# Optimization experiments

Hardware: AMD Instinct MI355X
Metric: run time of the kernel (lower is better)

Reference implementation:

```python
import jax, jax.numpy as jnp
import numpy as np
from jax import lax

DN = ('NCHW', 'OIHW', 'NCHW')

def conv2d(x, w, b, stride):
    y = lax.conv_general_dilated(x, w, (stride, stride), [(1, 1), (1, 1)], dimension_numbers=DN)
    return y + b[None, :, None, None]

def conv_transpose2d(x, w, b):
    # PyTorch ConvTranspose2d(k=3, stride=2, padding=1, output_padding=1)
    # == conv with lhs_dilation=2, pad low = k-1-p = 1, pad high = k-1-p+op = 2,
    # kernel spatially flipped and in/out channel dims swapped.  w: [in, out, kh, kw]
    wf = jnp.flip(w, (2, 3)).transpose(1, 0, 2, 3)  # [out, in, kh, kw]
    y = lax.conv_general_dilated(x, wf, (1, 1), [(1, 2), (1, 2)], lhs_dilation=(2, 2), dimension_numbers=DN)
    return y + b[None, :, None, None]

def setup_inputs() -> dict:
    key = jax.random.key(0)
    ks = jax.random.split(key, 20)
    s = 0.05
    inp = {
        'x':   jax.random.normal(ks[0], (64, 2, 256, 256), jnp.float32),
        'w1':  jax.random.normal(ks[1], (32, 2, 3, 3), jnp.float32) * s,
        'b1':  jnp.zeros((32,), jnp.float32),
        'w2':  jax.random.normal(ks[2], (64, 32, 3, 3), jnp.float32) * s,
        'b2':  jnp.zeros((64,), jnp.float32),
        'w3':  jax.random.normal(ks[3], (128, 64, 3, 3), jnp.float32) * s,
        'b3':  jnp.zeros((128,), jnp.float32),
        'w4':  jax.random.normal(ks[4], (128, 128, 3, 3), jnp.float32) * s,
        'b4':  jnp.zeros((128,), jnp.float32),
        'emb': jax.random.normal(ks[5], (512, 64), jnp.float32) * s,
        'dw1': jax.random.normal(ks[6], (128, 64, 3, 3), jnp.float32) * s,   # ConvTranspose2d weight [in, out, kh, kw]
        'db1': jnp.zeros((64,), jnp.float32),
        'dw2': jax.random.normal(ks[7], (64, 32, 3, 3), jnp.float32) * s,
        'db2': jnp.zeros((32,), jnp.float32),
        'dw3': jax.random.normal(ks[8], (32, 1, 3, 3), jnp.float32) * s,
        'db3': jnp.zeros((1,), jnp.float32),
    }
    return inp

def reference(x, w1, b1, w2, b2, w3, b3, w4, b4, emb, dw1, db1, dw2, db2, dw3, db3):
    # ---- Encoder ----
    h = jax.nn.relu(conv2d(x, w1, b1, 2))
    h = jax.nn.relu(conv2d(h, w2, b2, 2))
    h = jax.nn.relu(conv2d(h, w3, b3, 2))
    encoded = jax.nn.relu(conv2d(h, w4, b4, 1))  # [B, 128, H/8, W/8]

    # ---- VectorQuantizerEMA (inference math: cdist + argmin + lookup, straight-through) ----
    D = emb.shape[1]  # 64
    flat = encoded.reshape(encoded.shape[0], encoded.shape[1], -1).reshape(-1, D)  # [N, 64]
    dist = (jnp.sum(flat * flat, axis=1, keepdims=True)
            - 2.0 * flat @ emb.T
            + jnp.sum(emb * emb, axis=1)[None, :])  # [N, 512]
    idx = jnp.argmin(dist, axis=1)  # [N]
    quantized = emb[idx]            # [N, 64] gather
    q_st = flat + lax.stop_gradient(quantized - flat)  # straight-through estimator
    vq_feature = q_st.reshape(encoded.shape)

    # ---- Decoder ----
    d = jax.nn.relu(conv_transpose2d(vq_feature, dw1, db1))
    d = jax.nn.relu(conv_transpose2d(d, dw2, db2))
    decoded = conv_transpose2d(d, dw3, db3)  # [B, 1, 256, 256]
    return decoded
```

## Files before the change

kernel.cpp:

```cpp
#include <hip/hip_runtime.h>


using short8  = __attribute__((ext_vector_type(8))) short;
using short4v = __attribute__((ext_vector_type(4))) short;
using floatx4 = __attribute__((ext_vector_type(4))) float;

__device__ inline unsigned short bf16rn(float f) {
  unsigned u = __float_as_uint(f);
  unsigned r = (u + 0x7fffu + ((u >> 16) & 1u)) >> 16;
  return (unsigned short)r;
}
__device__ inline float bf2f1(short h) {
  return __uint_as_float(((unsigned)(unsigned short)h) << 16);
}

__device__ const int DKY[9]  = {1, 1, 1, 2, 0, 2, 2, 0, 0};
__device__ const int DKX[9]  = {1, 2, 0, 1, 1, 2, 0, 2, 0};

__global__ __launch_bounds__(256) void ring_zero(short* __restrict__ h,
                                                 short* __restrict__ l,
                                                 int nimg, int PH, int PW, int C) {
  const int RC = (2 * PW + 2 * (PH - 2)) * C;
  int t = blockIdx.x * 256 + threadIdx.x;
  if (t >= nimg * RC) return;
  const int nl = t / RC;
  int rem = t - nl * RC;
  const int p = rem / C;
  const int ch = rem - p * C;
  int r, c;
  if (p < 2 * PW) {
    r = (p < PW) ? 0 : PH - 1;
    c = (p < PW) ? p : p - PW;
  } else {
    int q = p - 2 * PW;
    if (q < PH - 2) { r = 1 + q; c = 0; }
    else { r = 1 + q - (PH - 2); c = PW - 1; }
  }
  const size_t a = (((size_t)nl * PH + r) * PW + c) * C + ch;
  h[a] = 0; l[a] = 0;
}

__global__ __launch_bounds__(256) void ring_zero1(short* __restrict__ h,
                                                  int nimg, int PH, int PW, int C) {
  const int RC = (2 * PW + 2 * (PH - 2)) * C;
  int t = blockIdx.x * 256 + threadIdx.x;
  if (t >= nimg * RC) return;
  const int nl = t / RC;
  int rem = t - nl * RC;
  const int p = rem / C;
  const int ch = rem - p * C;
  int r, c;
  if (p < 2 * PW) {
    r = (p < PW) ? 0 : PH - 1;
    c = (p < PW) ? p : p - PW;
  } else {
    int q = p - 2 * PW;
    if (q < PH - 2) { r = 1 + q; c = 0; }
    else { r = 1 + q - (PH - 2); c = PW - 1; }
  }
  h[(((size_t)nl * PH + r) * PW + c) * C + ch] = 0;
}

__global__ __launch_bounds__(256) void conv1_xt(const float* __restrict__ x,
                                                const float* __restrict__ w,
                                                const float* __restrict__ bias,
                                                short* __restrict__ oh,
                                                short* __restrict__ ol, int NH) {
  int t = blockIdx.x * 256 + threadIdx.x;
  if (t >= NH * 128 * 128) return;
  const int px = t & 16383;
  const int n  = t >> 14;
  const int r = px >> 7, c = px & 127;
  const int ih0 = 2 * r - 1, iw0 = 2 * c - 1;
  float acc[32];
#pragma unroll
  for (int o = 0; o < 32; ++o) acc[o] = bias[o];
  const float* ip = x + (size_t)n * 2 * 65536;
#pragma unroll
  for (int ic = 0; ic < 2; ++ic, ip += 65536) {
    float v[9];
#pragma unroll
    for (int kh = 0; kh < 3; ++kh) {
      const int ih = ih0 + kh;
#pragma unroll
      for (int kw = 0; kw < 3; ++kw) {
        const int iw = iw0 + kw;
        const bool ok = (ih >= 0) && (ih < 256) && (iw >= 0) && (iw < 256);
        v[kh * 3 + kw] = ok ? ip[ih * 256 + iw] : 0.f;
      }
    }
#pragma unroll
    for (int o = 0; o < 32; ++o) {
      float s = acc[o];
#pragma unroll
      for (int k = 0; k < 9; ++k) s = fmaf(v[k], w[(o * 2 + ic) * 9 + k], s);
      acc[o] = s;
    }
  }
  const size_t base = (((size_t)n * 130 + r + 1) * 130 + (c + 1)) * 32;
  short8 vh[4], vl[4];
#pragma unroll
  for (int g = 0; g < 4; ++g) {
#pragma unroll
    for (int kk = 0; kk < 8; ++kk) {
      const float rv = fmaxf(acc[g * 8 + kk], 0.f);
      const unsigned short hh = bf16rn(rv);
      vh[g][kk] = (short)hh;
      vl[g][kk] = (short)bf16rn(rv - __uint_as_float((unsigned)hh << 16));
    }
    *(short8*)(oh + base + g * 8) = vh[g];
    *(short8*)(ol + base + g * 8) = vl[g];
  }
}

template<int CIN, int COUT>
__global__ __launch_bounds__(256) void wprep_conv(const float* __restrict__ w,
                                                  short* __restrict__ hi,
                                                  short* __restrict__ lo) {
  constexpr int MT = COUT / 16;
  const int t = blockIdx.x * 256 + threadIdx.x;
  const int j = t & 7;
  const int lane = (t >> 3) & 63;
  const int g = t >> 9;
  const int mt = g % MT;
  const int s = g / MT;
  const int icb = s / 9, tap = s - icb * 9;
  const int kh = tap / 3, kw = tap - kh * 3;
  const int m = mt * 16 + (lane & 15);
  const int ic = icb * 32 + ((lane >> 4) << 3) + j;
  const float v = w[((m * CIN + ic) * 3 + kh) * 3 + kw];
  const unsigned short h = bf16rn(v);
  hi[t] = (short)h;
  lo[t] = (short)bf16rn(v - __uint_as_float((unsigned)h << 16));
}

template<int CIN, int COUT>
__global__ __launch_bounds__(256) void wprep_dec_h(const float* __restrict__ w,
                                                   short* __restrict__ hi) {
  constexpr int MT = COUT / 16, ICB = CIN / 32;
  const int t = blockIdx.x * 256 + threadIdx.x;
  const int j = t & 7;
  const int lane = (t >> 3) & 63;
  const int g = t >> 9;
  const int mt = g % MT;
  const int u = g / MT;
  const int icb = u % ICB;
  const int e = u / ICB;
  const int ky = DKY[e], kx = DKX[e];
  const int m = mt * 16 + (lane & 15);
  const int ic = icb * 32 + ((lane >> 4) << 3) + j;
  hi[t] = (short)bf16rn(w[((ic * COUT + m) * 3 + ky) * 3 + kx]);
}

template<int CIN, int COUT, int OH, int OW, int S, int PHI, int PWI, int PHO, int PWO, int NP>
__global__ __launch_bounds__(256) void conv_mfma_xt(
    const short* __restrict__ xih, const short* __restrict__ xil,
    const short* __restrict__ ah,  const short* __restrict__ al,
    const float* __restrict__ bias,
    short* __restrict__ xoh, short* __restrict__ xol) {
  constexpr int MT = COUT / 16, ICB = CIN / 32;
  constexpr int PXB = 64 * NP, TPB = OH * OW / PXB;
  const int b = blockIdx.x;
  const int n = b / TPB, pt = b % TPB;
  const int lane = threadIdx.x & 63, wave = threadIdx.x >> 6;
  const int quad = lane >> 4;
  int rr[NP], cc[NP];
  size_t bbase[NP];
#pragma unroll
  for (int p = 0; p < NP; ++p) {
    const int pl = pt * PXB + wave * (16 * NP) + p * 16 + (lane & 15);
    rr[p] = pl / OW; cc[p] = pl % OW;
    bbase[p] = (((size_t)n * PHI + S * rr[p]) * PWI + S * cc[p]) * CIN + quad * 8;
  }

  floatx4 acc[MT][NP];
#pragma unroll
  for (int mt = 0; mt < MT; ++mt)
#pragma unroll
    for (int p = 0; p < NP; ++p) acc[mt][p] = (floatx4){0.f, 0.f, 0.f, 0.f};

  const short8* __restrict__ ah8 = (const short8*)ah;
  const short8* __restrict__ al8 = (const short8*)al;

  for (int icb = 0; icb < ICB; ++icb) {
#pragma unroll
    for (int tap = 0; tap < 9; ++tap) {
      const int kh = tap / 3, kw = tap - kh * 3;
      short8 bh[NP], bl[NP];
#pragma unroll
      for (int p = 0; p < NP; ++p) {
        const size_t be = bbase[p] + (size_t)(kh * PWI + kw) * CIN + icb * 32;
        bh[p] = *(const short8*)(xih + be);
        bl[p] = *(const short8*)(xil + be);
      }
#pragma unroll
      for (int mt = 0; mt < MT; ++mt) {
        const int fi = ((icb * 9 + tap) * MT + mt) * 64 + lane;
        const short8 wh = ah8[fi];
        const short8 wl = al8[fi];
#pragma unroll
        for (int p = 0; p < NP; ++p) {
          acc[mt][p] = __builtin_amdgcn_mfma_f32_16x16x32_bf16(wh, bh[p], acc[mt][p], 0, 0, 0);
          acc[mt][p] = __builtin_amdgcn_mfma_f32_16x16x32_bf16(wh, bl[p], acc[mt][p], 0, 0, 0);
          acc[mt][p] = __builtin_amdgcn_mfma_f32_16x16x32_bf16(wl, bh[p], acc[mt][p], 0, 0, 0);
        }
      }
    }
  }
#pragma unroll
  for (int p = 0; p < NP; ++p) {
    const size_t ob = (((size_t)n * PHO + rr[p] + 1) * PWO + (cc[p] + 1)) * COUT + quad * 4;
#pragma unroll
    for (int mt = 0; mt < MT; ++mt) {
      short4v sh, sl;
#pragma unroll
      for (int q = 0; q < 4; ++q) {
        const float v = fmaxf(acc[mt][p][q] + bias[mt * 16 + quad * 4 + q], 0.f);
        const unsigned short hh = bf16rn(v);
        sh[q] = (short)hh;
        sl[q] = (short)bf16rn(v - __uint_as_float((unsigned)hh << 16));
      }
      *(short4v*)(xoh + ob + mt * 16) = sh;
      *(short4v*)(xol + ob + mt * 16) = sl;
    }
  }
}

template<int CIN, int COUT, int IH, int IW, int PHI, int PWI, int PHO, int PWO, int NP>
__global__ __launch_bounds__(256) void deconv_bf16_xt(
    const short* __restrict__ xih, const short* __restrict__ ah,
    const float* __restrict__ bias, short* __restrict__ xoh) {
  constexpr int MT = COUT / 16, ICB = CIN / 32;
  constexpr int PXB = 64 * NP, TPB = IH * IW / PXB;
  constexpr int PHE[9] = {0, 1, 1, 2, 2, 3, 3, 3, 3};
  constexpr int DE[9]  = {0, 0, 1, 0, 2, 0, 1, 2, 3};
  const int b = blockIdx.x;
  const int n = b / TPB, pt = b % TPB;
  const int lane = threadIdx.x & 63, wave = threadIdx.x >> 6;
  const int quad = lane >> 4;
  int ii[NP], jj[NP];
  size_t p00[NP];
#pragma unroll
  for (int p = 0; p < NP; ++p) {
    const int pl = pt * PXB + wave * (16 * NP) + p * 16 + (lane & 15);
    ii[p] = pl / IW; jj[p] = pl % IW;
    p00[p] = (((size_t)n * PHI + (ii[p] + 1)) * PWI + (jj[p] + 1)) * CIN + quad * 8;
  }

  floatx4 acc[4][MT][NP];
#pragma unroll
  for (int ph = 0; ph < 4; ++ph)
#pragma unroll
    for (int mt = 0; mt < MT; ++mt)
#pragma unroll
      for (int p = 0; p < NP; ++p) acc[ph][mt][p] = (floatx4){0.f, 0.f, 0.f, 0.f};

  const short8* __restrict__ ah8 = (const short8*)ah;
  for (int icb = 0; icb < ICB; ++icb) {
    short8 bh[NP][4];
#pragma unroll
    for (int p = 0; p < NP; ++p)
#pragma unroll
      for (int d = 0; d < 4; ++d)
        bh[p][d] = *(const short8*)(xih + p00[p] +
                                    (size_t)((d >> 1) * PWI + (d & 1)) * CIN + icb * 32);
#pragma unroll
    for (int e = 0; e < 9; ++e) {
      const int ph = PHE[e], d = DE[e];
#pragma unroll
      for (int mt = 0; mt < MT; ++mt) {
        const short8 wh = ah8[((e * ICB + icb) * MT + mt) * 64 + lane];
#pragma unroll
        for (int p = 0; p < NP; ++p)
          acc[ph][mt][p] = __builtin_amdgcn_mfma_f32_16x16x32_bf16(
              wh, bh[p][d], acc[ph][mt][p], 0, 0, 0);
      }
    }
  }
#pragma unroll
  for (int p = 0; p < NP; ++p)
#pragma unroll
    for (int ph = 0; ph < 4; ++ph) {
      const int oy = 2 * ii[p] + (ph >> 1), ox = 2 * jj[p] + (ph & 1);
      const size_t ob = (((size_t)n * PHO + oy + 1) * PWO + (ox + 1)) * COUT + quad * 4;
#pragma unroll
      for (int mt = 0; mt < MT; ++mt) {
        short4v sh;
#pragma unroll
        for (int q = 0; q < 4; ++q)
          sh[q] = (short)bf16rn(fmaxf(acc[ph][mt][p][q] + bias[mt * 16 + quad * 4 + q], 0.f));
        *(short4v*)(xoh + ob + mt * 16) = sh;
      }
    }
}

__global__ __launch_bounds__(256) void conv4_mfma(
    const short* __restrict__ xthi, const short* __restrict__ xtlo,
    const short* __restrict__ ahi,  const short* __restrict__ alo,
    const float* __restrict__ bias,
    short* __restrict__ ench, short* __restrict__ encl) {
  __shared__ short lh[6 * 34 * 32];
  __shared__ short ll[6 * 34 * 32];
  const int b    = blockIdx.x;
  const int n    = b >> 3;
  const int pt   = b & 7;
  const int r0   = pt * 4;
  const int lane = threadIdx.x & 63;
  const int wave = threadIdx.x >> 6;
  const int kq   = lane >> 4;
  int pl[2], lrow[2], lcol[2];
#pragma unroll
  for (int p = 0; p < 2; ++p) {
    pl[p] = pt * 128 + wave * 32 + p * 16 + (lane & 15);
    lrow[p] = (pl[p] >> 5) - r0;
    lcol[p] = pl[p] & 31;
  }

  floatx4 acc[8][2];
#pragma unroll
  for (int mt = 0; mt < 8; ++mt)
#pragma unroll
    for (int p = 0; p < 2; ++p) acc[mt][p] = (floatx4){0.f, 0.f, 0.f, 0.f};

  const short8* __restrict__ ah8 = (const short8*)ahi;
  const short8* __restrict__ al8 = (const short8*)alo;
  const short* __restrict__ ghbase = xthi + (((size_t)n * 34 + r0) * 34) * 128;
  const short* __restrict__ glbase = xtlo + (((size_t)n * 34 + r0) * 34) * 128;

  int s = 0;
  for (int icb = 0; icb < 4; ++icb) {
    __syncthreads();
    {
      const short* gh = ghbase + icb * 32;
      const short* gl = glbase + icb * 32;
      for (int t = threadIdx.x; t < 816; t += 256) {
        const int wr  = t * 8;
        const int row = wr / 1088;
        const int rem = wr - row * 1088;
        const int col = rem >> 5;
        const int ch  = rem & 31;
        const size_t g = ((size_t)(row * 34 + col)) * 128 + ch;
        *(short8*)(lh + wr) = *(const short8*)(gh + g);
        *(short8*)(ll + wr) = *(const short8*)(gl + g);
      }
    }
    __syncthreads();
#pragma unroll
    for (int tap = 0; tap < 9; ++tap, ++s) {
      const int kh = tap / 3, kw = tap - kh * 3;
      short8 bh[2], bl[2];
#pragma unroll
      for (int p = 0; p < 2; ++p) {
        const int le = ((lrow[p] + kh) * 34 + (lcol[p] + kw)) * 32 + kq * 8;
        bh[p] = *(const short8*)(lh + le);
        bl[p] = *(const short8*)(ll + le);
      }
#pragma unroll
      for (int mt = 0; mt < 8; ++mt) {
        const int fi = ((s * 8 + mt) << 6) + lane;
        const short8 ah = ah8[fi];
        const short8 al = al8[fi];
#pragma unroll
        for (int p = 0; p < 2; ++p) {
          acc[mt][p] = __builtin_amdgcn_mfma_f32_16x16x32_bf16(ah, bh[p], acc[mt][p], 0, 0, 0);
          acc[mt][p] = __builtin_amdgcn_mfma_f32_16x16x32_bf16(ah, bl[p], acc[mt][p], 0, 0, 0);
          acc[mt][p] = __builtin_amdgcn_mfma_f32_16x16x32_bf16(al, bh[p], acc[mt][p], 0, 0, 0);
        }
      }
    }
  }
#pragma unroll
  for (int p = 0; p < 2; ++p) {
    const size_t obase = (size_t)n * 128 * 1024 + pl[p];
#pragma unroll
    for (int mt = 0; mt < 8; ++mt) {
#pragma unroll
      for (int q = 0; q < 4; ++q) {
        const int cout = mt * 16 + kq * 4 + q;
        const float rr = fmaxf(acc[mt][p][q] + bias[cout], 0.f);
        const unsigned short h = bf16rn(rr);
        const size_t oi = obase + (size_t)cout * 1024;
        ench[oi] = (short)h;
        encl[oi] = (short)bf16rn(rr - __uint_as_float((unsigned)h << 16));
      }
    }
  }
}

__global__ __launch_bounds__(256) void vq_norms(const float* __restrict__ emb,
                                                float* __restrict__ norms) {
  int jj = blockIdx.x * 256 + threadIdx.x;
  if (jj < 512) {
    float s = 0.f;
    const float* e = emb + jj * 64;
#pragma unroll
    for (int k = 0; k < 64; ++k) s = fmaf(e[k], e[k], s);
    norms[jj] = s;
  }
}

__global__ __launch_bounds__(256) void emb_prep(const float* __restrict__ emb,
                                                short* __restrict__ hi,
                                                short* __restrict__ lo) {
  const int t = blockIdx.x * 256 + threadIdx.x;
  const int j  = t & 7;
  const int l  = (t >> 3) & 63;
  const int kk = (t >> 9) & 1;
  const int ct = t >> 10;
  const int code = ct * 16 + (l & 15);
  const int k = kk * 32 + ((l >> 4) << 3) + j;
  const float v = emb[code * 64 + k];
  const unsigned short h = bf16rn(v);
  hi[t] = (short)h;
  lo[t] = (short)bf16rn(v - __uint_as_float((unsigned)h << 16));
}

__global__ __launch_bounds__(256) void vq_mfma(
    const short* __restrict__ fhi, const short* __restrict__ flo,
    const short* __restrict__ ebh, const short* __restrict__ ebl,
    const float* __restrict__ nrm, const float* __restrict__ emb,
    short* __restrict__ d1h) {
  __shared__ int sidx[64];
  const int lane = threadIdx.x & 63;
  const int wave = threadIdx.x >> 6;
  const int r0 = blockIdx.x * 64 + wave * 16;
  const size_t abase = ((size_t)(r0 + (lane & 15))) * 64 + ((lane >> 4) << 3);
  short8 ah0 = *(const short8*)(fhi + abase);
  short8 ah1 = *(const short8*)(fhi + abase + 32);
  short8 al0 = *(const short8*)(flo + abase);
  short8 al1 = *(const short8*)(flo + abase + 32);

  float bestv[4] = {3.4e38f, 3.4e38f, 3.4e38f, 3.4e38f};
  int   besti[4] = {0, 0, 0, 0};
  const short8* __restrict__ ebh8 = (const short8*)ebh;
  const short8* __restrict__ ebl8 = (const short8*)ebl;
  for (int ct = 0; ct < 32; ++ct) {
    const int f0 = (ct * 2) * 64 + lane;
    const short8 b0h = ebh8[f0];
    const short8 b1h = ebh8[f0 + 64];
    const short8 b0l = ebl8[f0];
    const short8 b1l = ebl8[f0 + 64];
    floatx4 acc = {0.f, 0.f, 0.f, 0.f};
    acc = __builtin_amdgcn_mfma_f32_16x16x32_bf16(ah0, b0h, acc, 0, 0, 0);
    acc = __builtin_amdgcn_mfma_f32_16x16x32_bf16(ah1, b1h, acc, 0, 0, 0);
    acc = __builtin_amdgcn_mfma_f32_16x16x32_bf16(ah0, b0l, acc, 0, 0, 0);
    acc = __builtin_amdgcn_mfma_f32_16x16x32_bf16(ah1, b1l, acc, 0, 0, 0);
    acc = __builtin_amdgcn_mfma_f32_16x16x32_bf16(al0, b0h, acc, 0, 0, 0);
    acc = __builtin_amdgcn_mfma_f32_16x16x32_bf16(al1, b1h, acc, 0, 0, 0);
    const int code = ct * 16 + (lane & 15);
    const float nn = nrm[code];
#pragma unroll
    for (int q = 0; q < 4; ++q) {
      const float sc = nn - 2.f * acc[q];
      if (sc < bestv[q]) { bestv[q] = sc; besti[q] = code; }
    }
  }
#pragma unroll
  for (int off = 1; off < 16; off <<= 1) {
#pragma unroll
    for (int q = 0; q < 4; ++q) {
      const float ov = __shfl_xor(bestv[q], off, 64);
      const int   oi = __shfl_xor(besti[q], off, 64);
      if (ov < bestv[q] || (ov == bestv[q] && oi < besti[q])) {
        bestv[q] = ov; besti[q] = oi;
      }
    }
  }
  if ((lane & 15) == 0) {
#pragma unroll
    for (int q = 0; q < 4; ++q)
      sidx[wave * 16 + (lane >> 4) * 4 + q] = besti[q];
  }
  __syncthreads();
  const int row  = threadIdx.x >> 2;
  const int part = threadIdx.x & 3;
  const int rid = blockIdx.x * 64 + row;
  const int n  = rid >> 11;
  const int ch = (rid >> 4) & 127;
  const int pb = rid & 15;
  const int gi = sidx[row];
  const float4* src = (const float4*)(emb + (size_t)gi * 64 + part * 16);
  float4 v0 = src[0], v1 = src[1], v2 = src[2], v3 = src[3];
  float vals[16] = {v0.x, v0.y, v0.z, v0.w, v1.x, v1.y, v1.z, v1.w,
                    v2.x, v2.y, v2.z, v2.w, v3.x, v3.y, v3.z, v3.w};
#pragma unroll
  for (int kk = 0; kk < 16; ++kk) {
    const int k = part * 16 + kk;
    const int pix = pb * 64 + k;
    const int r = pix >> 5, c = pix & 31;
    const size_t a = (((size_t)n * 34 + r + 1) * 34 + (c + 1)) * 128 + ch;
    d1h[a] = (short)bf16rn(vals[kk]);
  }
}

__global__ __launch_bounds__(256) void dec3_xt(const short* __restrict__ xh,
                                               const float* __restrict__ w,
                                               const float* __restrict__ bias,
                                               float* __restrict__ out, int NH) {
  int t = blockIdx.x * 256 + threadIdx.x;
  if (t >= NH * 128 * 128) return;
  const int px = t & 16383;
  const int nl = t >> 14;
  const int i = px >> 7, j = px & 127;
  const float b0 = bias[0];
  float a00 = b0, a01 = b0, a10 = b0, a11 = b0;
  const size_t base00 = (((size_t)nl * 130 + i + 1) * 130 + (j + 1)) * 32;
#pragma unroll
  for (int icg = 0; icg < 4; ++icg) {
    const short8 h00 = *(const short8*)(xh + base00 + icg * 8);
    const short8 h01 = *(const short8*)(xh + base00 + 32 + icg * 8);
    const short8 h10 = *(const short8*)(xh + base00 + 130 * 32 + icg * 8);
    const short8 h11 = *(const short8*)(xh + base00 + 130 * 32 + 32 + icg * 8);
#pragma unroll
    for (int kk = 0; kk < 8; ++kk) {
      const int ic = icg * 8 + kk;
      const float x00 = bf2f1(h00[kk]);
      const float x01 = bf2f1(h01[kk]);
      const float x10 = bf2f1(h10[kk]);
      const float x11 = bf2f1(h11[kk]);
      const float* wp = w + ic * 9;
      a00 = fmaf(x00, wp[4], a00);
      a01 = fmaf(x00, wp[5], fmaf(x01, wp[3], a01));
      a10 = fmaf(x00, wp[7], fmaf(x10, wp[1], a10));
      a11 = fmaf(x00, wp[8], fmaf(x01, wp[6], fmaf(x10, wp[2], fmaf(x11, wp[0], a11))));
    }
  }
  float* op = out + ((size_t)nl * 256 + 2 * i) * 256 + 2 * j;
  op[0] = a00; op[1] = a01; op[256] = a10; op[257] = a11;
}

extern "C" void kernel_launch(void* const* d_in, const int* in_sizes, int n_in,
                              void* d_out, int out_size, void* d_ws, size_t ws_size,
                              hipStream_t stream) {
  const float* x   = (const float*)d_in[0];
  const float* w1  = (const float*)d_in[1];
  const float* b1  = (const float*)d_in[2];
  const float* w2  = (const float*)d_in[3];
  const float* b2  = (const float*)d_in[4];
  const float* w3  = (const float*)d_in[5];
  const float* b3  = (const float*)d_in[6];
  const float* w4  = (const float*)d_in[7];
  const float* b4  = (const float*)d_in[8];
  const float* emb = (const float*)d_in[9];
  const float* dw1 = (const float*)d_in[10];
  const float* db1 = (const float*)d_in[11];
  const float* dw2 = (const float*)d_in[12];
  const float* db2 = (const float*)d_in[13];
  const float* dw3 = (const float*)d_in[14];
  const float* db3 = (const float*)d_in[15];
  float* outp = (float*)d_out;

  const int N = in_sizes[0] / (2 * 256 * 256);
  if (N & 1) return;
  const int NH = N / 2;

  const size_t sx3 = (size_t)N * 66 * 66 * 64;
  const size_t sx2 = (size_t)NH * 130 * 130 * 32;
  const size_t sx4 = (size_t)N * 34 * 34 * 128;
  const size_t se  = (size_t)N * 128 * 1024;
  const size_t sd1 = sx4;
  const size_t smalls = 512 + 18432 + 73728 + 147456 + 73728 + 18432 + 32768;
  const size_t need = (sx3 + sx4 + se + sd1 + smalls) * sizeof(float);
  if (ws_size < need) return;

  float* ws = (float*)d_ws;
  short* x3h = (short*)ws;                 short* x3l = x3h + sx3;
  short* x2h = (short*)(ws + sx3);         short* x2l = x2h + sx2;
  short* x4h = (short*)(ws + sx3);         short* x4l = x4h + sx4;
  short* ech = (short*)(ws + sx3 + sx4);   short* ecl = ech + se;
  short* d1h = (short*)(ws + sx3 + sx4 + se);
  short* d2h = (short*)ws;
  short* d3h = (short*)(ws + sx3);
  float* sm  = ws + sx3 + sx4 + se + sd1;
  float* nrm = sm;
  short* a2h = (short*)(sm + 512);                         short* a2l = a2h + 18432;
  short* a3h = (short*)(sm + 512 + 18432);                 short* a3l = a3h + 73728;
  short* a4h = (short*)(sm + 512 + 18432 + 73728);         short* a4l = a4h + 147456;
  short* ad1h = (short*)(sm + 512 + 18432 + 73728 + 147456);
  short* ad2h = (short*)(sm + 512 + 18432 + 73728 + 147456 + 73728);
  short* ebh = (short*)(sm + 512 + 18432 + 73728 + 147456 + 73728 + 18432); short* ebl = ebh + 32768;

  wprep_conv<32, 64><<<72, 256, 0, stream>>>(w2, a2h, a2l);
  wprep_conv<64, 128><<<288, 256, 0, stream>>>(w3, a3h, a3l);
  wprep_conv<128, 128><<<576, 256, 0, stream>>>(w4, a4h, a4l);
  wprep_dec_h<128, 64><<<288, 256, 0, stream>>>(dw1, ad1h);
  wprep_dec_h<64, 32><<<72, 256, 0, stream>>>(dw2, ad2h);
  vq_norms<<<2, 256, 0, stream>>>(emb, nrm);
  emb_prep<<<128, 256, 0, stream>>>(emb, ebh, ebl);

  ring_zero<<<(int)((NH * 516 * 32 + 255) / 256), 256, 0, stream>>>(x2h, x2l, NH, 130, 130, 32);
  ring_zero<<<(int)(((size_t)N * 260 * 64 + 255) / 256), 256, 0, stream>>>(x3h, x3l, N, 66, 66, 64);
  for (int half = 0; half < 2; ++half) {
    const int n0 = half * NH;
    conv1_xt<<<NH * 16384 / 256, 256, 0, stream>>>(
        x + (size_t)n0 * 2 * 65536, w1, b1, x2h, x2l, NH);
    conv_mfma_xt<32, 64, 64, 64, 2, 130, 130, 66, 66, 2>
        <<<NH * 32, 256, 0, stream>>>(x2h, x2l, a2h, a2l, b2,
                                      x3h + (size_t)n0 * 66 * 66 * 64,
                                      x3l + (size_t)n0 * 66 * 66 * 64);
  }
  ring_zero<<<(int)(((size_t)N * 132 * 128 + 255) / 256), 256, 0, stream>>>(x4h, x4l, N, 34, 34, 128);
  conv_mfma_xt<64, 128, 32, 32, 2, 66, 66, 34, 34, 2>
      <<<N * 8, 256, 0, stream>>>(x3h, x3l, a3h, a3l, b3, x4h, x4l);
  conv4_mfma<<<N * 8, 256, 0, stream>>>(x4h, x4l, a4h, a4l, b4, ech, ecl);

  ring_zero1<<<(int)(((size_t)N * 132 * 128 + 255) / 256), 256, 0, stream>>>(d1h, N, 34, 34, 128);
  vq_mfma<<<N * 2048 / 64, 256, 0, stream>>>(ech, ecl, ebh, ebl, nrm, emb, d1h);

  ring_zero1<<<(int)(((size_t)N * 260 * 64 + 255) / 256), 256, 0, stream>>>(d2h, N, 66, 66, 64);
  deconv_bf16_xt<128, 64, 32, 32, 34, 34, 66, 66, 2>
      <<<N * 8, 256, 0, stream>>>(d1h, ad1h, db1, d2h);
  ring_zero1<<<(int)((NH * 516 * 32 + 255) / 256), 256, 0, stream>>>(d3h, NH, 130, 130, 32);
  for (int half = 0; half < 2; ++half) {
    const int n0 = half * NH;
    deconv_bf16_xt<64, 32, 64, 64, 66, 66, 130, 130, 2>
        <<<NH * 32, 256, 0, stream>>>(d2h + (size_t)n0 * 66 * 66 * 64,
                                      ad2h, db2, d3h);
    dec3_xt<<<NH * 16384 / 256, 256, 0, stream>>>(
        d3h, dw3, db3, outp + (size_t)n0 * 65536, NH);
  }
}
```

Measured before the change: 651.2 us.

## Double-buffer conv4 LDS tiles and split output channels across twice the waves

The conv4 kernel now runs with 512 threads, so each pair of waves shares a pixel group and each wave computes half of the output-channel tiles. This halves the accumulator registers per wave. The shared-memory input tile is double-buffered: the next channel block is prefetched into registers while MFMAs run on the current buffer, and it is stored to LDS afterward, leaving one barrier per iteration. The goal is to hide global load latency and raise occupancy, at the cost of twice the LDS and of redundant B-fragment LDS reads, since both channel halves load the same pixels.

```diff
diff --git a/kernel.cpp b/kernel.cpp
--- a/kernel.cpp
+++ b/kernel.cpp
@@ -294,31 +294,34 @@
     }
 }
 
-__global__ __launch_bounds__(256) void conv4_mfma(
+__global__ __launch_bounds__(512, 4) void conv4_mfma(
     const short* __restrict__ xthi, const short* __restrict__ xtlo,
     const short* __restrict__ ahi,  const short* __restrict__ alo,
     const float* __restrict__ bias,
     short* __restrict__ ench, short* __restrict__ encl) {
-  __shared__ short lh[6 * 34 * 32];
-  __shared__ short ll[6 * 34 * 32];
+  __shared__ short lh[2][6 * 34 * 32];
+  __shared__ short ll[2][6 * 34 * 32];
   const int b    = blockIdx.x;
   const int n    = b >> 3;
   const int pt   = b & 7;
   const int r0   = pt * 4;
-  const int lane = threadIdx.x & 63;
-  const int wave = threadIdx.x >> 6;
+  const int tid  = threadIdx.x;
+  const int lane = tid & 63;
+  const int wave = tid >> 6;
+  const int pw   = wave >> 1;
+  const int cs   = wave & 1;
   const int kq   = lane >> 4;
   int pl[2], lrow[2], lcol[2];
 #pragma unroll
   for (int p = 0; p < 2; ++p) {
-    pl[p] = pt * 128 + wave * 32 + p * 16 + (lane & 15);
+    pl[p] = pt * 128 + pw * 32 + p * 16 + (lane & 15);
     lrow[p] = (pl[p] >> 5) - r0;
     lcol[p] = pl[p] & 31;
   }
 
-  floatx4 acc[8][2];
-#pragma unroll
-  for (int mt = 0; mt < 8; ++mt)
+  floatx4 acc[4][2];
+#pragma unroll
+  for (int mt = 0; mt < 4; ++mt)
 #pragma unroll
     for (int p = 0; p < 2; ++p) acc[mt][p] = (floatx4){0.f, 0.f, 0.f, 0.f};
 
@@ -327,24 +330,43 @@
   const short* __restrict__ ghbase = xthi + (((size_t)n * 34 + r0) * 34) * 128;
   const short* __restrict__ glbase = xtlo + (((size_t)n * 34 + r0) * 34) * 128;
 
+  const int t0 = tid, t1 = tid + 512;
+  size_t g0 = 0, g1 = 0;
+  {
+    const int wr0 = t0 * 8, row0 = wr0 / 1088, rem0 = wr0 - row0 * 1088;
+    g0 = ((size_t)(row0 * 34 + (rem0 >> 5))) * 128 + (rem0 & 31);
+    const int wr1 = t1 * 8, row1 = wr1 / 1088, rem1 = wr1 - row1 * 1088;
+    g1 = ((size_t)(row1 * 34 + (rem1 >> 5))) * 128 + (rem1 & 31);
+  }
+  short8 rh0, rl0, rh1, rl1;
+
+  rh0 = *(const short8*)(ghbase + g0);
+  rl0 = *(const short8*)(glbase + g0);
+  if (t1 < 816) {
+    rh1 = *(const short8*)(ghbase + g1);
+    rl1 = *(const short8*)(glbase + g1);
+  }
+  *(short8*)(lh[0] + t0 * 8) = rh0;
+  *(short8*)(ll[0] + t0 * 8) = rl0;
+  if (t1 < 816) {
+    *(short8*)(lh[1 - 1] + t1 * 8) = rh1;
+    *(short8*)(ll[1 - 1] + t1 * 8) = rl1;
+  }
+  __syncthreads();
+
   int s = 0;
   for (int icb = 0; icb < 4; ++icb) {
-    __syncthreads();
-    {
-      const short* gh = ghbase + icb * 32;
-      const short* gl = glbase + icb * 32;
-      for (int t = threadIdx.x; t < 816; t += 256) {
-        const int wr  = t * 8;
-        const int row = wr / 1088;
-        const int rem = wr - row * 1088;
-        const int col = rem >> 5;
-        const int ch  = rem & 31;
-        const size_t g = ((size_t)(row * 34 + col)) * 128 + ch;
-        *(short8*)(lh + wr) = *(const short8*)(gh + g);
-        *(short8*)(ll + wr) = *(const short8*)(gl + g);
-      }
-    }
-    __syncthreads();
+    if (icb < 3) {
+      const size_t off = (size_t)(icb + 1) * 32;
+      rh0 = *(const short8*)(ghbase + off + g0);
+      rl0 = *(const short8*)(glbase + off + g0);
+      if (t1 < 816) {
+        rh1 = *(const short8*)(ghbase + off + g1);
+        rl1 = *(const short8*)(glbase + off + g1);
+      }
+    }
+    const short* __restrict__ lhc = lh[icb & 1];
+    const short* __restrict__ llc = ll[icb & 1];
 #pragma unroll
     for (int tap = 0; tap < 9; ++tap, ++s) {
       const int kh = tap / 3, kw = tap - kh * 3;
@@ -352,12 +374,13 @@
 #pragma unroll
       for (int p = 0; p < 2; ++p) {
         const int le = ((lrow[p] + kh) * 34 + (lcol[p] + kw)) * 32 + kq * 8;
-        bh[p] = *(const short8*)(lh + le);
-        bl[p] = *(const short8*)(ll + le);
-      }
-#pragma unroll
-      for (int mt = 0; mt < 8; ++mt) {
-        const int fi = ((s * 8 + mt) << 6) + lane;
+        bh[p] = *(const short8*)(lhc + le);
+        bl[p] = *(const short8*)(llc + le);
+      }
+#pragma unroll
+      for (int mt = 0; mt < 4; ++mt) {
+        const int mtg = cs * 4 + mt;
+        const int fi = ((s * 8 + mtg) << 6) + lane;
         const short8 ah = ah8[fi];
         const short8 al = al8[fi];
 #pragma unroll
@@ -368,15 +391,26 @@
         }
       }
     }
+    if (icb < 3) {
+      const int nb = (icb + 1) & 1;
+      *(short8*)(lh[nb] + t0 * 8) = rh0;
+      *(short8*)(ll[nb] + t0 * 8) = rl0;
+      if (t1 < 816) {
+        *(short8*)(lh[nb] + t1 * 8) = rh1;
+        *(short8*)(ll[nb] + t1 * 8) = rl1;
+      }
+      __syncthreads();
+    }
   }
 #pragma unroll
   for (int p = 0; p < 2; ++p) {
     const size_t obase = (size_t)n * 128 * 1024 + pl[p];
 #pragma unroll
-    for (int mt = 0; mt < 8; ++mt) {
+    for (int mt = 0; mt < 4; ++mt) {
+      const int mtg = cs * 4 + mt;
 #pragma unroll
       for (int q = 0; q < 4; ++q) {
-        const int cout = mt * 16 + kq * 4 + q;
+        const int cout = mtg * 16 + kq * 4 + q;
         const float rr = fmaxf(acc[mt][p][q] + bias[cout], 0.f);
         const unsigned short h = bf16rn(rr);
         const size_t oi = obase + (size_t)cout * 1024;
@@ -602,7 +636,7 @@
   ring_zero<<<(int)(((size_t)N * 132 * 128 + 255) / 256), 256, 0, stream>>>(x4h, x4l, N, 34, 34, 128);
   conv_mfma_xt<64, 128, 32, 32, 2, 66, 66, 34, 34, 2>
       <<<N * 8, 256, 0, stream>>>(x3h, x3l, a3h, a3l, b3, x4h, x4l);
-  conv4_mfma<<<N * 8, 256, 0, stream>>>(x4h, x4l, a4h, a4l, b4, ech, ecl);
+  conv4_mfma<<<N * 8, 512, 0, stream>>>(x4h, x4l, a4h, a4l, b4, ech, ecl);
 
   ring_zero1<<<(int)(((size_t)N * 132 * 128 + 255) / 256), 256, 0, stream>>>(d1h, N, 34, 34, 128);
   vq_mfma<<<N * 2048 / 64, 256, 0, stream>>>(ech, ecl, ebh, ebl, nrm, emb, d1h);
```

Measured after the change: 675.8 us. 3.8% more time.
